# Performance work log

Hardware: AMD Instinct MI355X
Metric: run time of the kernel (lower is better)

## Reference

```python
import jax, jax.numpy as jnp
import numpy as np

B, S, D_IN, H, NH, L = 8, 1024, 512, 1024, 16, 4
HD = H // NH
SCALE = HD ** -0.5
EPS = 1e-5


def _ln(x, g, b):
    m = jnp.mean(x, axis=-1, keepdims=True)
    v = jnp.mean((x - m) ** 2, axis=-1, keepdims=True)
    return (x - m) * jax.lax.rsqrt(v + EPS) * g + b


def setup_inputs() -> dict:
    key = jax.random.key(0)
    ks = jax.random.split(key, 12)
    s = lambda k, shape, fan: jax.random.normal(k, shape, jnp.float32) * (fan ** -0.5)
    return {
        "x": jax.random.normal(ks[0], (B, S, D_IN), jnp.float32),
        "W_in": s(ks[1], (D_IN, H), D_IN), "b_in": jnp.zeros((H,), jnp.float32),
        "W_qkv": s(ks[2], (L, H, 3 * H), H), "b_qkv": jnp.zeros((L, 3 * H), jnp.float32),
        "W_o": s(ks[3], (L, H, H), H), "b_o": jnp.zeros((L, H), jnp.float32),
        "g1": jnp.ones((L, H), jnp.float32), "be1": jnp.zeros((L, H), jnp.float32),
        "W_out": s(ks[4], (H, H), H), "b_out": jnp.zeros((H,), jnp.float32),
        "g2": jnp.ones((H,), jnp.float32), "be2": jnp.zeros((H,), jnp.float32),
    }


def _attn_layer(x, Wqkv, bqkv, Wo, bo, g, be):
    b, s, h = x.shape
    qkv = (x @ Wqkv + bqkv).reshape(b, s, 3, NH, HD)
    q = qkv[:, :, 0].transpose(0, 2, 1, 3)  # [B,NH,S,HD]
    k = qkv[:, :, 1].transpose(0, 2, 1, 3)
    v = qkv[:, :, 2].transpose(0, 2, 1, 3)
    scores = jnp.einsum("bhqd,bhkd->bhqk", q, k) * SCALE
    w = jax.nn.softmax(scores, axis=-1)  # dropout is identity in eval
    o = jnp.einsum("bhqk,bhkd->bhqd", w, v)
    o = o.transpose(0, 2, 1, 3).reshape(b, s, h)
    return _ln(o @ Wo + bo + x, g, be)


def reference(x, W_in, b_in, W_qkv, b_qkv, W_o, b_o, g1, be1, W_out, b_out, g2, be2):
    h = x @ W_in + b_in
    for i in range(L):
        h = _attn_layer(h, W_qkv[i], b_qkv[i], W_o[i], b_o[i], g1[i], be1[i])
    pooled = jnp.mean(h, axis=1)  # [B,H]
    return _ln(pooled @ W_out + b_out, g2, be2)
```

## Files before the change

### kernel.cpp

```cpp
#include <hip/hip_runtime.h>
#include <stdint.h>

typedef unsigned short u16;
typedef unsigned int   u32;
typedef __attribute__((ext_vector_type(8))) short short8;
typedef __attribute__((ext_vector_type(4))) float f32x4;
typedef __attribute__((ext_vector_type(16))) float f32x16;
typedef __attribute__((ext_vector_type(2))) unsigned int uint2v;

#define B_   8
#define S_   1024
#define DIN_ 512
#define H_   1024
#define NH_  16
#define HD_  64
#define L_   4
#define M_   (B_*S_)
#define SCALE_ 0.125f
#define EPS_ 1e-5f

__device__ __forceinline__ u16 f2b(float f) {
  u32 u = __builtin_bit_cast(u32, f);
  u32 r = (u + 0x7fffu + ((u >> 16) & 1u)) >> 16;
  return (u16)r;
}

__device__ __forceinline__ u32 cvtpk(float lo, float hi) {
  u32 r;
  asm("v_cvt_pk_bf16_f32 %0, %1, %2" : "=v"(r) : "v"(lo), "v"(hi));
  return r;
}

__device__ __forceinline__ void gll16(const void* g, void* l) {
  __builtin_amdgcn_global_load_lds(
      (const __attribute__((address_space(1))) u32*)(uintptr_t)g,
      (__attribute__((address_space(3))) u32*)(uintptr_t)l,
      16, 0, 0);
}

__global__ void cvt_k(const float* __restrict__ in, u16* __restrict__ out) {
  long i = (long)(blockIdx.x * 256 + threadIdx.x) * 4;
  f32x4 v = *(const f32x4*)&in[i];
  u32 p0 = (u32)f2b(v[0]) | ((u32)f2b(v[1]) << 16);
  u32 p1 = (u32)f2b(v[2]) | ((u32)f2b(v[3]) << 16);
  u32* o = (u32*)&out[i];
  o[0] = p0; o[1] = p1;
}

__global__ __launch_bounds__(256)
void tcvt_k(const float* __restrict__ in0, u16* __restrict__ out0, int R, int C) {
  __shared__ float t[32][33];
  const float* in = in0 + (size_t)blockIdx.z * R * C;
  u16* out = out0 + (size_t)blockIdx.z * R * C;
  int tx = threadIdx.x & 31, ty = threadIdx.x >> 5;
  long r0 = blockIdx.y * 32, c0 = blockIdx.x * 32;
#pragma unroll
  for (int i = 0; i < 4; ++i)
    t[ty + i*8][tx] = in[(r0 + ty + i*8) * (long)C + c0 + tx];
  __syncthreads();
#pragma unroll
  for (int i = 0; i < 4; ++i)
    out[(c0 + ty + i*8) * (long)R + r0 + tx] = f2b(t[tx][ty + i*8]);
}

template<int EPI>
__global__ __launch_bounds__(256, 2)
void gemm_k(const u16* __restrict__ A, const u16* __restrict__ Bt,
            const float* __restrict__ bias,
            float* __restrict__ Cf, u16* __restrict__ Cb,
            const float* __restrict__ Res,
            int Ndim, int K, int scale_cols)
{
  __shared__ u16 As[128 * 32];
  __shared__ u16 Bs[128 * 32];
  const int tid = threadIdx.x;
  const int lane = tid & 63;
  const int wid = tid >> 6;
  const int wr = wid >> 1, wc = wid & 1;
  const int l15 = lane & 15, l4 = lane >> 4;
  const long arow0 = (long)blockIdx.x * 128;
  const long brow0 = (long)blockIdx.y * 128;

  f32x4 acc[4][4] = {};

  const int srow = tid >> 2;
  const int scol = (tid & 3) * 8;
  const u16* ga  = A  + (arow0 + srow) * K + scol;
  const u16* ga1 = ga + 64 * (long)K;
  const u16* gb  = Bt + (brow0 + srow) * K + scol;
  const u16* gb1 = gb + 64 * (long)K;
  u16* lA0 = &As[tid * 8];
  u16* lA1 = &As[2048 + tid * 8];
  u16* lB0 = &Bs[tid * 8];
  u16* lB1 = &Bs[2048 + tid * 8];

  for (int k0 = 0; k0 < K; k0 += 32) {
    gll16(ga + k0, lA0);
    gll16(ga1 + k0, lA1);
    gll16(gb + k0, lB0);
    gll16(gb1 + k0, lB1);
    __syncthreads();
    short8 af[4], bf[4];
#pragma unroll
    for (int m = 0; m < 4; ++m)
      af[m] = *(const short8*)&As[(wr*64 + m*16 + l15) * 32 + l4*8];
#pragma unroll
    for (int n = 0; n < 4; ++n)
      bf[n] = *(const short8*)&Bs[(wc*64 + n*16 + l15) * 32 + l4*8];
#pragma unroll
    for (int m = 0; m < 4; ++m)
#pragma unroll
      for (int n = 0; n < 4; ++n)
        acc[m][n] = __builtin_amdgcn_mfma_f32_16x16x32_bf16(af[m], bf[n], acc[m][n], 0, 0, 0);
    __syncthreads();
  }

  const int crow = wr*64 + l4*4;
  const int ccol = wc*64 + l15;
#pragma unroll
  for (int m = 0; m < 4; ++m) {
#pragma unroll
    for (int n = 0; n < 4; ++n) {
      const int col = (int)brow0 + ccol + n*16;
      const float bv = bias[col];
      const float sc = (EPI == 1 && col < scale_cols) ? SCALE_ : 1.0f;
#pragma unroll
      for (int r = 0; r < 4; ++r) {
        const long row = arow0 + crow + m*16 + r;
        float v = acc[m][n][r] + bv;
        if (EPI == 1) {
          Cb[row * Ndim + col] = f2b(v * sc);
        } else if (EPI == 0) {
          Cf[row * Ndim + col] = v;
          Cb[row * Ndim + col] = f2b(v);
        } else {
          Cf[row * Ndim + col] = v + Res[row * Ndim + col];
        }
      }
    }
  }
}

__global__ __launch_bounds__(512)
void attn_k(const u16* __restrict__ qkv, u16* __restrict__ ob)
{
  __shared__ u16 Ks[2][4096];
  __shared__ u16 Vs[2][4096];

  const int tid = threadIdx.x, lane = tid & 63, wid = tid >> 6;
  const int l31 = lane & 31, hi = lane >> 5;

  const int blk = blockIdx.x;
  const int xcd = blk & 7, slot = blk >> 3;
  const int bh = xcd + ((slot >> 2) << 3);
  const int qx = slot & 3;
  const int b = bh >> 4, nh = bh & 15;
  const int q0 = qx * 256 + wid * 32;

  const int RS = 3 * H_;
  const long base = (long)b * S_ * RS;
  const u16* Qg = qkv + base + nh * HD_;
  const u16* Kg = qkv + base + H_ + nh * HD_;
  const u16* Vg = qkv + base + 2 * H_ + nh * HD_;

  short8 qf[4];
#pragma unroll
  for (int ks = 0; ks < 4; ++ks)
    qf[ks] = *(const short8*)&Qg[(long)(q0 + l31) * RS + ks*16 + hi*8];

  float m_ = -1e30f, l_ = 0.f;
  f32x16 o0 = {}, o1 = {};

  const int krow = tid >> 3, kc = tid & 7;
  const int ksc = kc ^ (krow & 7);
  const long kgoff = (long)krow * RS + ksc * 8;
  const int vd = tid & 63, vch = tid >> 6;
  const int vbyt = (vd*128 + vch*16) ^ ((vd & 7) << 4);

  {
    gll16(Kg + kgoff, (char*)&Ks[0][0] + tid*16);
    union { u16 u[8]; short8 v; } tv;
#pragma unroll
    for (int j = 0; j < 8; ++j)
      tv.u[j] = Vg[(long)(vch*8 + j) * RS + vd];
    *(short8*)((char*)&Vs[0][0] + vbyt) = tv.v;
  }
  __syncthreads();

  for (int t = 0; t < 16; ++t) {
    const int cur = t & 1, nxt = cur ^ 1;
    union { u16 u[8]; short8 v; } ta;
    if (t < 15) {
      const long kv1 = (long)(t + 1) * 64;
      gll16(Kg + kv1 * RS + kgoff, (char*)&Ks[nxt][0] + tid*16);
#pragma unroll
      for (int j = 0; j < 8; ++j)
        ta.u[j] = Vg[(kv1 + vch*8 + j) * RS + vd];
    }

    f32x16 s0 = {}, s1 = {};
    __builtin_amdgcn_s_setprio(1);
#pragma unroll
    for (int ks = 0; ks < 4; ++ks) {
      const int koff = ks*32 + hi*16;
      const int by0 = (l31*128 + koff) ^ ((l31 & 7) << 4);
      short8 kf0 = *(const short8*)((const char*)&Ks[cur][0] + by0);
      s0 = __builtin_amdgcn_mfma_f32_32x32x16_bf16(kf0, qf[ks], s0, 0, 0, 0);
      const int by1 = ((32 + l31)*128 + koff) ^ ((l31 & 7) << 4);
      short8 kf1 = *(const short8*)((const char*)&Ks[cur][0] + by1);
      s1 = __builtin_amdgcn_mfma_f32_32x32x16_bf16(kf1, qf[ks], s1, 0, 0, 0);
    }
    __builtin_amdgcn_s_setprio(0);

    float tmax = -1e30f;
#pragma unroll
    for (int r = 0; r < 16; ++r) tmax = fmaxf(tmax, fmaxf(s0[r], s1[r]));
    tmax = fmaxf(tmax, __shfl_xor(tmax, 32));
    if (!__all(tmax <= m_ + 8.f)) {
      const float mnew = fmaxf(m_, tmax);
      const float corr = __expf(m_ - mnew);
      m_ = mnew; l_ *= corr;
#pragma unroll
      for (int r = 0; r < 16; ++r) {
        float cr = __shfl(corr, (r&3) + 8*(r>>2) + 4*hi);
        o0[r] *= cr; o1[r] *= cr;
      }
    }
    float sum = 0.f;
#pragma unroll
    for (int r = 0; r < 16; ++r) {
      float p0 = __expf(s0[r] - m_);
      float p1 = __expf(s1[r] - m_);
      s0[r] = p0; s1[r] = p1;
      sum += p0 + p1;
    }
    sum += __shfl_xor(sum, 32);
    l_ += sum;

    short8 pa[4];
#pragma unroll
    for (int ks2 = 0; ks2 < 2; ++ks2) {
      const int r0 = 8 * ks2;
      u32 A0 = cvtpk(s0[r0+0], s0[r0+1]), A1 = cvtpk(s0[r0+2], s0[r0+3]);
      u32 B0 = cvtpk(s0[r0+4], s0[r0+5]), B1 = cvtpk(s0[r0+6], s0[r0+7]);
      uint2v w02 = __builtin_amdgcn_permlane32_swap(A0, B0, false, false);
      uint2v w13 = __builtin_amdgcn_permlane32_swap(A1, B1, false, false);
      union { u32 w[4]; short8 v; } u_;
      u_.w[0] = w02.x; u_.w[1] = w13.x; u_.w[2] = w02.y; u_.w[3] = w13.y;
      pa[ks2] = u_.v;
    }
#pragma unroll
    for (int ks2 = 0; ks2 < 2; ++ks2) {
      const int r0 = 8 * ks2;
      u32 A0 = cvtpk(s1[r0+0], s1[r0+1]), A1 = cvtpk(s1[r0+2], s1[r0+3]);
      u32 B0 = cvtpk(s1[r0+4], s1[r0+5]), B1 = cvtpk(s1[r0+6], s1[r0+7]);
      uint2v w02 = __builtin_amdgcn_permlane32_swap(A0, B0, false, false);
      uint2v w13 = __builtin_amdgcn_permlane32_swap(A1, B1, false, false);
      union { u32 w[4]; short8 v; } u_;
      u_.w[0] = w02.x; u_.w[1] = w13.x; u_.w[2] = w02.y; u_.w[3] = w13.y;
      pa[2 + ks2] = u_.v;
    }

    __builtin_amdgcn_s_setprio(1);
#pragma unroll
    for (int ks = 0; ks < 4; ++ks) {
      const int vb = ks*32 + hi*16;
      const int by0 = (l31*128 + vb) ^ ((l31 & 7) << 4);
      short8 v0 = *(const short8*)((const char*)&Vs[cur][0] + by0);
      o0 = __builtin_amdgcn_mfma_f32_32x32x16_bf16(pa[ks], v0, o0, 0, 0, 0);
      const int by1 = ((32 + l31)*128 + vb) ^ ((l31 & 7) << 4);
      short8 v1 = *(const short8*)((const char*)&Vs[cur][0] + by1);
      o1 = __builtin_amdgcn_mfma_f32_32x32x16_bf16(pa[ks], v1, o1, 0, 0, 0);
    }
    __builtin_amdgcn_s_setprio(0);

    if (t < 15) {
      *(short8*)((char*)&Vs[nxt][0] + vbyt) = ta.v;
      __syncthreads();
    }
  }

  const float linv = 1.0f / l_;
#pragma unroll
  for (int r = 0; r < 16; ++r) {
    const int rowq = (r&3) + 8*(r>>2) + 4*hi;
    const float li = __shfl(linv, rowq);
    const long srow = (long)(b * S_ + q0 + rowq);
    ob[srow * H_ + nh*HD_ + l31]      = f2b(o0[r] * li);
    ob[srow * H_ + nh*HD_ + 32 + l31] = f2b(o1[r] * li);
  }
}

__global__ __launch_bounds__(256)
void ln_k(const float* __restrict__ in, const float* __restrict__ g,
          const float* __restrict__ be, float* __restrict__ outf,
          u16* __restrict__ outb)
{
  const int row = blockIdx.x;
  const int tid = threadIdx.x;
  const float* x = in + (long)row * H_;
  f32x4 v = *(const f32x4*)&x[tid * 4];
  float s  = v[0] + v[1] + v[2] + v[3];
  float ss = v[0]*v[0] + v[1]*v[1] + v[2]*v[2] + v[3]*v[3];
#pragma unroll
  for (int o = 1; o < 64; o <<= 1) {
    s  += __shfl_xor(s, o);
    ss += __shfl_xor(ss, o);
  }
  __shared__ float rs[4], rq[4];
  const int wid = tid >> 6;
  if ((tid & 63) == 0) { rs[wid] = s; rq[wid] = ss; }
  __syncthreads();
  float ts = rs[0] + rs[1] + rs[2] + rs[3];
  float tq = rq[0] + rq[1] + rq[2] + rq[3];
  const float mu = ts * (1.0f / H_);
  const float var = tq * (1.0f / H_) - mu * mu;
  const float rstd = rsqrtf(var + EPS_);
  const long obase = (long)row * H_ + tid * 4;
#pragma unroll
  for (int j = 0; j < 4; ++j) {
    int c = tid * 4 + j;
    float y = (v[j] - mu) * rstd * g[c] + be[c];
    outf[obase + j] = y;
    if (outb) outb[obase + j] = f2b(y);
  }
}

__global__ void pool_k(const float* __restrict__ hf, float* __restrict__ pooled) {
  const int c = blockIdx.x * 256 + threadIdx.x;
  const int b = blockIdx.y;
  const int s0 = blockIdx.z * 128;
  float s = 0.f;
  for (int t = 0; t < 128; ++t) s += hf[((long)(b * S_ + s0 + t)) * H_ + c];
  atomicAdd(&pooled[b * H_ + c], s * (1.0f / S_));
}

__global__ void fgemm_k(const float* __restrict__ pooled, const float* __restrict__ W,
                        const float* __restrict__ bias, float* __restrict__ out) {
  const int n = blockIdx.x * 256 + threadIdx.x;
  const int b = blockIdx.y;
  float s = bias[n];
  for (int k = 0; k < H_; ++k) s += pooled[b * H_ + k] * W[(long)k * H_ + n];
  out[b * H_ + n] = s;
}

extern "C" void kernel_launch(void* const* d_in, const int* in_sizes, int n_in,
                              void* d_out, int out_size, void* d_ws, size_t ws_size,
                              hipStream_t stream) {
  const float* x     = (const float*)d_in[0];
  const float* W_in  = (const float*)d_in[1];
  const float* b_in  = (const float*)d_in[2];
  const float* W_qkv = (const float*)d_in[3];
  const float* b_qkv = (const float*)d_in[4];
  const float* W_o   = (const float*)d_in[5];
  const float* b_o   = (const float*)d_in[6];
  const float* g1    = (const float*)d_in[7];
  const float* be1   = (const float*)d_in[8];
  const float* W_out = (const float*)d_in[9];
  const float* b_out = (const float*)d_in[10];
  const float* g2    = (const float*)d_in[11];
  const float* be2   = (const float*)d_in[12];
  float* outp = (float*)d_out;

  char* ws = (char*)d_ws;
  float* hf    = (float*)(ws + 0);
  u16*   hb    = (u16*)(ws + 33554432);
  u16*   qkvb  = (u16*)(ws + 50331648);
  float* resf  = (float*)(ws + 50331648);
  u16*   ob    = (u16*)(ws + 100663296);
  u16*   xb    = (u16*)(ws + 100663296);
  u16*   WinT  = (u16*)(ws + 117440512);
  u16*   WqkvT = (u16*)(ws + 118489088);
  u16*   WoT   = (u16*)(ws + 143654912);
  float* pooled= (float*)(ws + 152043520);
  float* tmpf  = (float*)(ws + 152076288);

  cvt_k<<<dim3(M_ * DIN_ / 1024), 256, 0, stream>>>(x, xb);
  tcvt_k<<<dim3(H_/32, DIN_/32, 1), 256, 0, stream>>>(W_in, WinT, DIN_, H_);
  tcvt_k<<<dim3(3*H_/32, H_/32, L_), 256, 0, stream>>>(W_qkv, WqkvT, H_, 3*H_);
  tcvt_k<<<dim3(H_/32, H_/32, L_), 256, 0, stream>>>(W_o, WoT, H_, H_);

  gemm_k<0><<<dim3(M_/128, H_/128), 256, 0, stream>>>(xb, WinT, b_in, hf, hb, nullptr, H_, DIN_, 0);

  for (int l = 0; l < L_; ++l) {
    gemm_k<1><<<dim3(M_/128, 3*H_/128), 256, 0, stream>>>(hb, WqkvT + (size_t)l*3*H_*H_,
                                                          b_qkv + l*3*H_, nullptr, qkvb, nullptr,
                                                          3*H_, H_, H_);
    attn_k<<<dim3(512), 512, 0, stream>>>(qkvb, ob);
    gemm_k<2><<<dim3(M_/128, H_/128), 256, 0, stream>>>(ob, WoT + (size_t)l*H_*H_,
                                                        b_o + l*H_, resf, nullptr, hf,
                                                        H_, H_, 0);
    ln_k<<<dim3(M_), 256, 0, stream>>>(resf, g1 + l*H_, be1 + l*H_, hf, hb);
  }

  hipMemsetAsync(pooled, 0, B_ * H_ * sizeof(float), stream);
  pool_k<<<dim3(H_/256, B_, 8), 256, 0, stream>>>(hf, pooled);
  fgemm_k<<<dim3(H_/256, B_), 256, 0, stream>>>(pooled, W_out, b_out, tmpf);
  ln_k<<<dim3(B_), 256, 0, stream>>>(tmpf, g2, be2, outp, nullptr);
}
```

Before: 951.6 us.

## Triple-buffer GEMM LDS tiles with async global loads and raised MFMA priority

The GEMM main loop now keeps three LDS buffers for the A and B tiles and issues global-to-LDS loads two k-steps ahead. It uses explicit vmcnt waits and barriers in place of a load-then-sync-then-compute sequence, so memory latency can overlap with MFMA work. It also raises wave priority around the MFMA block. The cost is three times the LDS per block, which may reduce occupancy under launch_bounds(256,2). The hand-written waitcnt counts and the barrier placement are also fragile to get right.

Measured after the change: 942.2 us. No clear change (-1.0%).

```diff
diff --git a/kernel.cpp b/kernel.cpp
--- a/kernel.cpp
+++ b/kernel.cpp
@@ -71,8 +71,8 @@
             const float* __restrict__ Res,
             int Ndim, int K, int scale_cols)
 {
-  __shared__ u16 As[128 * 32];
-  __shared__ u16 Bs[128 * 32];
+  __shared__ u16 As[3][128 * 32];
+  __shared__ u16 Bs[3][128 * 32];
   const int tid = threadIdx.x;
   const int lane = tid & 63;
   const int wid = tid >> 6;
@@ -89,30 +89,45 @@
   const u16* ga1 = ga + 64 * (long)K;
   const u16* gb  = Bt + (brow0 + srow) * K + scol;
   const u16* gb1 = gb + 64 * (long)K;
-  u16* lA0 = &As[tid * 8];
-  u16* lA1 = &As[2048 + tid * 8];
-  u16* lB0 = &Bs[tid * 8];
-  u16* lB1 = &Bs[2048 + tid * 8];
-
-  for (int k0 = 0; k0 < K; k0 += 32) {
-    gll16(ga + k0, lA0);
-    gll16(ga1 + k0, lA1);
-    gll16(gb + k0, lB0);
-    gll16(gb1 + k0, lB1);
-    __syncthreads();
+
+  auto STAGE = [&](int buf, int k0) {
+    gll16(ga + k0,  &As[buf][tid * 8]);
+    gll16(ga1 + k0, &As[buf][2048 + tid * 8]);
+    gll16(gb + k0,  &Bs[buf][tid * 8]);
+    gll16(gb1 + k0, &Bs[buf][2048 + tid * 8]);
+  };
+  auto COMPUTE = [&](int buf) {
     short8 af[4], bf[4];
 #pragma unroll
     for (int m = 0; m < 4; ++m)
-      af[m] = *(const short8*)&As[(wr*64 + m*16 + l15) * 32 + l4*8];
+      af[m] = *(const short8*)&As[buf][(wr*64 + m*16 + l15) * 32 + l4*8];
 #pragma unroll
     for (int n = 0; n < 4; ++n)
-      bf[n] = *(const short8*)&Bs[(wc*64 + n*16 + l15) * 32 + l4*8];
+      bf[n] = *(const short8*)&Bs[buf][(wc*64 + n*16 + l15) * 32 + l4*8];
+    __builtin_amdgcn_s_setprio(1);
 #pragma unroll
     for (int m = 0; m < 4; ++m)
 #pragma unroll
       for (int n = 0; n < 4; ++n)
         acc[m][n] = __builtin_amdgcn_mfma_f32_16x16x32_bf16(af[m], bf[n], acc[m][n], 0, 0, 0);
-    __syncthreads();
+    __builtin_amdgcn_s_setprio(0);
+  };
+
+  const int nt = K >> 5;
+  STAGE(0, 0);
+  STAGE(1, 32);
+  for (int t = 0; t < nt; ++t) {
+    if (t + 2 < nt) {
+      STAGE((t + 2) % 3, (t + 2) * 32);
+      asm volatile("s_waitcnt vmcnt(8)\n\ts_barrier" ::: "memory");
+    } else if (t + 1 < nt) {
+      asm volatile("s_waitcnt vmcnt(4)\n\ts_barrier" ::: "memory");
+    } else {
+      asm volatile("s_waitcnt vmcnt(0)\n\ts_barrier" ::: "memory");
+    }
+    COMPUTE(t % 3);
+    if (t + 1 < nt)
+      asm volatile("s_barrier" ::: "memory");
   }
 
   const int crow = wr*64 + l4*4;
```

## Add 256x256 eight-wave pipelined GEMM kernel for QKV projection

Applied to the files above, without the earlier changes.

Replaces the 128x128 generic GEMM used for the QKV projection with a dedicated 256x256-tile, 512-thread kernel. It uses an 8-phase software pipeline over double-buffered, XOR-swizzled LDS with direct global-to-LDS loads, and XCD-aware block swizzling. The intent is more data reuse per tile and better overlap of loads with MFMA work. In exchange it uses 128KB of LDS and many accumulator registers at one block per CU, and has fewer blocks (384) to fill the device.

Result: no change. 935.4 us (-1.7%).

```diff
diff --git a/kernel.cpp b/kernel.cpp
--- a/kernel.cpp
+++ b/kernel.cpp
@@ -141,6 +141,125 @@
   }
 }
 
+__global__ __launch_bounds__(512, 1)
+void gemm8_k(const u16* __restrict__ A, const u16* __restrict__ Bt,
+             const float* __restrict__ bias, u16* __restrict__ Cb)
+{
+  constexpr int K = 1024, N = 3 * H_;
+  constexpr int NT = K / 64;
+  __shared__ u16 lds[8][8192];
+
+  const int tid = threadIdx.x;
+  const int lane = tid & 63;
+  const int wid = tid >> 6;
+  const int wm = wid >> 2, wn = wid & 3;
+  const int l15 = lane & 15, l4 = lane >> 4;
+
+  const int bid = blockIdx.x;
+  const int swz = (bid & 7) * 48 + (bid >> 3);
+  const long arow0 = (long)(swz & 31) * 256;
+  const long brow0 = (long)(swz >> 5) * 256;
+
+  f32x4 acc[8][4] = {};
+  short8 bfr[4][2];
+  short8 afr[2][2];
+
+  auto stage = [&](int buf, int op, int half, int kt) {
+    const u16* src = op ? Bt : A;
+    const long rb = (op ? brow0 : arow0) + half * 128;
+    u16* dst = lds[buf*4 + op*2 + half];
+#pragma unroll
+    for (int ld = 0; ld < 2; ++ld) {
+      int p = ld * 512 + tid;
+      int row = p >> 3;
+      int kc = (p & 7) ^ (row & 7);
+      gll16(src + (rb + row) * (long)K + kt * 64 + kc * 8, (char*)dst + p * 16);
+    }
+  };
+  auto readB = [&](int buf) {
+    const char* base = (const char*)lds[buf*4 + 2 + (wn >> 1)];
+#pragma unroll
+    for (int n = 0; n < 4; ++n)
+#pragma unroll
+      for (int ks = 0; ks < 2; ++ks) {
+        int rh = (wn & 1) * 64 + n * 16 + l15;
+        int byt = rh * 128 + ((((ks*4 + l4) * 16)) ^ ((rh & 7) << 4));
+        bfr[n][ks] = *(const short8*)(base + byt);
+      }
+  };
+  auto readA = [&](int buf, int q) {
+    const char* base = (const char*)lds[buf*4 + wm];
+#pragma unroll
+    for (int j = 0; j < 2; ++j)
+#pragma unroll
+      for (int ks = 0; ks < 2; ++ks) {
+        int rh = (2*q + j) * 16 + l15;
+        int byt = rh * 128 + ((((ks*4 + l4) * 16)) ^ ((rh & 7) << 4));
+        afr[j][ks] = *(const short8*)(base + byt);
+      }
+  };
+  auto mm = [&](int q) {
+    __builtin_amdgcn_s_setprio(1);
+#pragma unroll
+    for (int j = 0; j < 2; ++j)
+#pragma unroll
+      for (int n = 0; n < 4; ++n)
+#pragma unroll
+        for (int ks = 0; ks < 2; ++ks)
+          acc[2*q+j][n] = __builtin_amdgcn_mfma_f32_16x16x32_bf16(
+              afr[j][ks], bfr[n][ks], acc[2*q+j][n], 0, 0, 0);
+    __builtin_amdgcn_s_setprio(0);
+  };
+
+#define PH(bufc, q, doB, sb, so, sh, st, doV)                     \
+    readA(bufc, q); if (doB) readB(bufc);                         \
+    stage(sb, so, sh, st);                                        \
+    __builtin_amdgcn_s_barrier();                                 \
+    asm volatile("s_waitcnt lgkmcnt(0)" ::: "memory");            \
+    __builtin_amdgcn_sched_barrier(0);                            \
+    mm(q);                                                        \
+    if (doV) asm volatile("s_waitcnt vmcnt(4)" ::: "memory");     \
+    __builtin_amdgcn_s_barrier();
+
+  stage(0,0,0,0); stage(0,0,1,0); stage(0,1,0,0); stage(0,1,1,0);
+  stage(1,1,0,1); stage(1,1,1,1);
+  asm volatile("s_waitcnt vmcnt(4)" ::: "memory");
+  __builtin_amdgcn_s_barrier();
+
+  const int niter = NT / 2;
+  for (int i = 0; i < niter; ++i) {
+    const int t1 = 2*i + 1;
+    const int t2 = (2*i + 2 < NT) ? 2*i + 2 : NT - 1;
+    const int t3 = (2*i + 3 < NT) ? 2*i + 3 : NT - 1;
+    PH(0, 0, true , 1, 0, 0, t1, false)
+    PH(0, 1, false, 1, 0, 1, t1, false)
+    PH(0, 2, false, 0, 1, 0, t2, false)
+    PH(0, 3, false, 0, 1, 1, t2, true )
+    PH(1, 0, true , 0, 0, 0, t2, false)
+    PH(1, 1, false, 0, 0, 1, t2, false)
+    PH(1, 2, false, 1, 1, 0, t3, false)
+    PH(1, 3, false, 1, 1, 1, t3, true )
+  }
+#undef PH
+
+  const long crow0 = arow0 + wm * 128;
+  const int  ccol0 = (int)brow0 + wn * 64;
+#pragma unroll
+  for (int m = 0; m < 8; ++m) {
+#pragma unroll
+    for (int n = 0; n < 4; ++n) {
+      const int col = ccol0 + n * 16 + l15;
+      const float bv = bias[col];
+      const float sc = (col < H_) ? SCALE_ : 1.0f;
+#pragma unroll
+      for (int r = 0; r < 4; ++r) {
+        const long row = crow0 + m * 16 + l4 * 4 + r;
+        Cb[row * N + col] = f2b((acc[m][n][r] + bv) * sc);
+      }
+    }
+  }
+}
+
 __global__ __launch_bounds__(512)
 void attn_k(const u16* __restrict__ qkv, u16* __restrict__ ob)
 {
@@ -383,9 +502,8 @@
   gemm_k<0><<<dim3(M_/128, H_/128), 256, 0, stream>>>(xb, WinT, b_in, hf, hb, nullptr, H_, DIN_, 0);
 
   for (int l = 0; l < L_; ++l) {
-    gemm_k<1><<<dim3(M_/128, 3*H_/128), 256, 0, stream>>>(hb, WqkvT + (size_t)l*3*H_*H_,
-                                                          b_qkv + l*3*H_, nullptr, qkvb, nullptr,
-                                                          3*H_, H_, H_);
+    gemm8_k<<<dim3((M_/256) * (3*H_/256)), 512, 0, stream>>>(hb, WqkvT + (size_t)l*3*H_*H_,
+                                                             b_qkv + l*3*H_, qkvb);
     attn_k<<<dim3(512), 512, 0, stream>>>(qkvb, ob);
     gemm_k<2><<<dim3(M_/128, H_/128), 256, 0, stream>>>(ob, WoT + (size_t)l*H_*H_,
                                                         b_o + l*H_, resf, nullptr, hf,
```
